# Optimization experiments

Measured on AMD Instinct MI355X. Metric: run time of the kernel, lower is better.

Reference implementation:

```python
import jax, jax.numpy as jnp
import numpy as np

B, L, HID, H, DH = 1, 2048, 1024, 16, 64
KW = 2  # d_conv
EPS = float(np.finfo(np.float32).eps)  # torch RMSNorm eps=None -> dtype eps


def _causal_dw_conv(x, w, b):
    # x: (B, L, D), w: (D, K), b: (D,). Depthwise causal conv, no activation.
    Bs, Ls, D = x.shape
    K = w.shape[1]
    xp = jnp.pad(x, ((0, 0), (K - 1, 0), (0, 0)))
    out = b
    for k in range(K):
        out = out + xp[:, k:k + Ls, :] * w[:, k]
    return out


def setup_inputs() -> dict:
    key = jax.random.key(0)
    ks = jax.random.split(key, 14)
    hidden_states = jax.random.normal(ks[0], (B, L, HID), jnp.float32)
    # masked_fill(attention_mask != 0, -inf): True above diagonal (future masked)
    attention_mask = jnp.triu(jnp.ones((L, L), dtype=bool), 1)[None, None]
    all_dim = 3 * H * DH  # q_size + 2*kv_size with KVH == H
    qkv_w = jax.random.normal(ks[1], (all_dim, HID), jnp.float32) * 0.02
    q_conv_w = jax.random.normal(ks[2], (H * DH, KW), jnp.float32) * 0.5
    q_conv_b = jax.random.normal(ks[3], (H * DH,), jnp.float32) * 0.02
    k_conv_w = jax.random.normal(ks[4], (H * DH, KW), jnp.float32) * 0.5
    k_conv_b = jax.random.normal(ks[5], (H * DH,), jnp.float32) * 0.02
    v_conv_w = jax.random.normal(ks[6], (H * DH, KW), jnp.float32) * 0.5
    v_conv_b = jax.random.normal(ks[7], (H * DH,), jnp.float32) * 0.02
    norm_w = jnp.ones((DH,), jnp.float32)
    A_log = jnp.log(jax.random.uniform(ks[8], (H,), jnp.float32, 1.0, 16.0))
    dt0 = jnp.exp(jax.random.uniform(ks[9], (H,), jnp.float32)
                  * (np.log(0.1) - np.log(0.001)) + np.log(0.001))
    dt0 = jnp.clip(dt0, 1e-4)
    dt_bias = dt0 + jnp.log(-jnp.expm1(-dt0))  # inverse softplus init
    dt_proj_w = jax.random.normal(ks[10], (H, HID), jnp.float32) * 0.02
    dt_proj_b = jnp.zeros((H,), jnp.float32)
    o_w = jax.random.normal(ks[11], (HID, H * DH), jnp.float32) * 0.02
    order_coeff = jnp.ones((1, H, 1, 1), jnp.float32)  # 1/cumprod(arange(1,2))
    return dict(hidden_states=hidden_states, attention_mask=attention_mask,
                qkv_w=qkv_w, q_conv_w=q_conv_w, q_conv_b=q_conv_b,
                k_conv_w=k_conv_w, k_conv_b=k_conv_b, v_conv_w=v_conv_w,
                v_conv_b=v_conv_b, norm_w=norm_w, A_log=A_log, dt_bias=dt_bias,
                dt_proj_w=dt_proj_w, dt_proj_b=dt_proj_b, o_w=o_w,
                order_coeff=order_coeff)


def reference(hidden_states, attention_mask, qkv_w, q_conv_w, q_conv_b,
              k_conv_w, k_conv_b, v_conv_w, v_conv_b, norm_w, A_log, dt_bias,
              dt_proj_w, dt_proj_b, o_w, order_coeff):
    qs = H * DH
    qkv = hidden_states @ qkv_w.T                    # (B, L, 3*H*DH)
    q = _causal_dw_conv(qkv[..., :qs], q_conv_w, q_conv_b)
    k = _causal_dw_conv(qkv[..., qs:2 * qs], k_conv_w, k_conv_b)
    v = _causal_dw_conv(qkv[..., 2 * qs:], v_conv_w, v_conv_b)
    # split heads -> (B, H, L, DH)
    q = q.reshape(B, L, H, DH).transpose(0, 2, 1, 3)
    k = k.reshape(B, L, H, DH).transpose(0, 2, 1, 3)
    v = v.reshape(B, L, H, DH).transpose(0, 2, 1, 3)
    # SSM-style gate: dt (B, L, H)
    dt = jax.nn.softplus(hidden_states @ dt_proj_w.T + dt_proj_b + dt_bias)
    v = v * jnp.swapaxes(dt, 1, 2)[..., None]        # value scaled by dt
    A = -jnp.exp(A_log)[None, None, :] * dt          # (B, L, H)
    A_cumsum = jnp.swapaxes(jnp.cumsum(A, axis=1), 1, 2)  # (B, H, L)
    diff = A_cumsum[:, :, :, None] - A_cumsum[:, :, None, :]  # (B, H, L, L)
    A_mask = jnp.exp(jnp.where(attention_mask, -jnp.inf, diff))
    # order == 1: Taylor series reduces to a single gated linear term
    scores = jnp.einsum('bhld,bhmd->bhlm', q, k) * A_mask * (1.0 / order_coeff)
    out = scores @ v                                  # (B, H, L, DH)
    # RMSNorm over head_dim
    out = out * jax.lax.rsqrt(jnp.mean(out * out, -1, keepdims=True) + EPS) * norm_w
    out = out.transpose(0, 2, 1, 3).reshape(B, L, H * DH)
    return out @ o_w.T
```

## Files before the change

### kernel.cpp

```cpp
#include <hip/hip_runtime.h>
#include <hip/hip_bf16.h>

#define L_SEQ 2048
#define HIDN  1024
#define NH    16
#define DHD   64
#define QKV_N 3072

typedef float f4 __attribute__((ext_vector_type(4)));
typedef __bf16 bf16x8 __attribute__((ext_vector_type(8)));
typedef _Float16 half8 __attribute__((ext_vector_type(8)));
typedef unsigned int u32x2 __attribute__((ext_vector_type(2)));

union H8 {
  half8 h;
  u32x2 u2[2];
  uint4 u4;
};

__device__ __forceinline__ float b2f(unsigned short u) {
  union { unsigned int i; float f; } c; c.i = ((unsigned int)u) << 16; return c.f;
}
__device__ __forceinline__ unsigned short f2b(float f) {
  union { float f; unsigned int i; } c; c.f = f;
  unsigned int r = c.i + 0x7FFFu + ((c.i >> 16) & 1u);
  return (unsigned short)(r >> 16);
}
__device__ __forceinline__ unsigned short f2h(float f) {
  union { _Float16 h; unsigned short u; } c; c.h = (_Float16)f; return c.u;
}
__device__ __forceinline__ void unpack8(uint4 u, float* f) {
  unsigned int w[4] = {u.x, u.y, u.z, u.w};
#pragma unroll
  for (int i = 0; i < 4; ++i) {
    union { unsigned int i_; float f_; } lo, hi;
    lo.i_ = w[i] << 16;
    hi.i_ = w[i] & 0xffff0000u;
    f[2 * i] = lo.f_; f[2 * i + 1] = hi.f_;
  }
}

__global__ void detect_kernel(const unsigned short* __restrict__ hs, int* flag) {
  __shared__ int cnt;
  if (threadIdx.x == 0) cnt = 0;
  __syncthreads();
  int c = 0;
  for (int i = threadIdx.x; i < 8192; i += 256) {
    unsigned int e = (hs[i] >> 7) & 0xFFu;
    if (e >= 140u) c++;
  }
  atomicAdd(&cnt, c);
  __syncthreads();
  if (threadIdx.x == 0) *flag = (cnt >= 32) ? 1 : 0;
}

__global__ __launch_bounds__(256) void convert_big(const void* __restrict__ in,
                                                   unsigned short* __restrict__ out,
                                                   int n, const int* __restrict__ flag) {
  const int i = (blockIdx.x * 256 + threadIdx.x) * 4;
  if (i >= n) return;
  if (*flag) {
    f4 v = *(const f4*)((const float*)in + i);
    ushort4 o;
    o.x = f2b(v[0]); o.y = f2b(v[1]); o.z = f2b(v[2]); o.w = f2b(v[3]);
    *(ushort4*)(out + i) = o;
  } else {
    *(uint2*)(out + i) = *(const uint2*)((const unsigned short*)in + i);
  }
}

__global__ __launch_bounds__(256) void convert_small(
    const void* qw, const void* qb, const void* kw, const void* kb,
    const void* vw, const void* vb, const void* nw, const void* al,
    const void* dtb, const void* dpb, const void* oc,
    float* __restrict__ out, const int* __restrict__ flag) {
  const int f = *flag;
  const void* ptrs[11] = {qw, qb, kw, kb, vw, vb, nw, al, dtb, dpb, oc};
  const int sizes[11] = {2048, 1024, 2048, 1024, 2048, 1024, 64, 16, 16, 16, 16};
  int off = 0;
  for (int a = 0; a < 11; ++a) {
    for (int i = threadIdx.x + blockIdx.x * 256; i < sizes[a]; i += gridDim.x * 256)
      out[off + i] = f ? ((const float*)ptrs[a])[i] : b2f(((const unsigned short*)ptrs[a])[i]);
    off += sizes[a];
  }
}

__global__ __launch_bounds__(256) void gemm128(
    const unsigned short* __restrict__ A, const unsigned short* __restrict__ B,
    float* __restrict__ C, int M, int N, int K)
{
  __shared__ __align__(16) unsigned short As[128 * 40];
  __shared__ __align__(16) unsigned short Bs[128 * 40];
  const int t = threadIdx.x;
  const int w = t >> 6, lane = t & 63;
  const int quad = lane >> 4, l16 = lane & 15;
  const int wr = w >> 1, wc = w & 1;
  const int m0 = blockIdx.y * 128, n0 = blockIdx.x * 128;
  const int srow = t >> 1;
  const int scol = (t & 1) * 16;

  f4 acc[4][4];
#pragma unroll
  for (int i = 0; i < 4; ++i)
#pragma unroll
    for (int j = 0; j < 4; ++j) acc[i][j] = (f4){0.f, 0.f, 0.f, 0.f};

  const unsigned short* apg = A + (size_t)(m0 + srow) * K + scol;
  const unsigned short* bpg = B + (size_t)(n0 + srow) * K + scol;
  uint4 a0 = *(const uint4*)apg,       a1 = *(const uint4*)(apg + 8);
  uint4 b0 = *(const uint4*)bpg,       b1 = *(const uint4*)(bpg + 8);

  for (int k0 = 0; k0 < K; k0 += 32) {
    __syncthreads();
    *(uint4*)&As[srow * 40 + scol]     = a0;
    *(uint4*)&As[srow * 40 + scol + 8] = a1;
    *(uint4*)&Bs[srow * 40 + scol]     = b0;
    *(uint4*)&Bs[srow * 40 + scol + 8] = b1;
    __syncthreads();
    if (k0 + 32 < K) {
      a0 = *(const uint4*)(apg + k0 + 32); a1 = *(const uint4*)(apg + k0 + 40);
      b0 = *(const uint4*)(bpg + k0 + 32); b1 = *(const uint4*)(bpg + k0 + 40);
    }
    bf16x8 aF[4], bF[4];
#pragma unroll
    for (int i = 0; i < 4; ++i)
      aF[i] = *(const bf16x8*)&As[(wr * 64 + i * 16 + l16) * 40 + quad * 8];
#pragma unroll
    for (int j = 0; j < 4; ++j)
      bF[j] = *(const bf16x8*)&Bs[(wc * 64 + j * 16 + l16) * 40 + quad * 8];
#pragma unroll
    for (int i = 0; i < 4; ++i)
#pragma unroll
      for (int j = 0; j < 4; ++j)
        acc[i][j] = __builtin_amdgcn_mfma_f32_16x16x32_bf16(aF[i], bF[j], acc[i][j], 0, 0, 0);
  }

#pragma unroll
  for (int i = 0; i < 4; ++i)
#pragma unroll
    for (int j = 0; j < 4; ++j)
#pragma unroll
      for (int r = 0; r < 4; ++r) {
        int m = m0 + wr * 64 + i * 16 + quad * 4 + r;
        int n = n0 + wc * 64 + j * 16 + l16;
        C[(size_t)m * N + n] = acc[i][j][r];
      }
}

template <int MODE>
__global__ __launch_bounds__(256) void gemm_bt(
    const unsigned short* __restrict__ A, const unsigned short* __restrict__ B,
    void* __restrict__ Cv, int M, int N, int K, const int* __restrict__ flag)
{
  __shared__ __align__(16) short As[64 * 40];
  __shared__ __align__(16) short Bs[64 * 40];
  const int t = threadIdx.x;
  const int wave = t >> 6, lane = t & 63;
  const int quad = lane >> 4, l16 = lane & 15;
  const int m0 = blockIdx.y * 64, n0 = blockIdx.x * 64;
  const int srow = t >> 2, scol = (t & 3) * 8;
  f4 acc[4];
#pragma unroll
  for (int i = 0; i < 4; ++i) acc[i] = (f4){0.f, 0.f, 0.f, 0.f};
  const unsigned short* ap = A + (size_t)(m0 + srow) * K + scol;
  const unsigned short* bp = B + (size_t)(n0 + srow) * K + scol;
  for (int k0 = 0; k0 < K; k0 += 32) {
    uint4 av = *(const uint4*)(ap + k0);
    uint4 bv = *(const uint4*)(bp + k0);
    __syncthreads();
    *(uint4*)&As[srow * 40 + scol] = av;
    *(uint4*)&Bs[srow * 40 + scol] = bv;
    __syncthreads();
    bf16x8 af = *(const bf16x8*)&As[(wave * 16 + l16) * 40 + quad * 8];
#pragma unroll
    for (int nt = 0; nt < 4; ++nt) {
      bf16x8 bf = *(const bf16x8*)&Bs[(nt * 16 + l16) * 40 + quad * 8];
      acc[nt] = __builtin_amdgcn_mfma_f32_16x16x32_bf16(af, bf, acc[nt], 0, 0, 0);
    }
  }
  const int outf32 = (MODE == 0) ? 1 : (*flag ? 1 : 0);
#pragma unroll
  for (int nt = 0; nt < 4; ++nt) {
#pragma unroll
    for (int r = 0; r < 4; ++r) {
      int m = m0 + wave * 16 + quad * 4 + r;
      int n = n0 + nt * 16 + l16;
      if (outf32) ((float*)Cv)[(size_t)m * N + n] = acc[nt][r];
      else        ((unsigned short*)Cv)[(size_t)m * N + n] = f2b(acc[nt][r]);
    }
  }
}

__global__ __launch_bounds__(256) void dt_kernel(
    const unsigned short* __restrict__ hs,
    const unsigned short* __restrict__ dtw,
    const float* __restrict__ smallf,
    float* __restrict__ dt_out, float* __restrict__ A_out)
{
  const int l = blockIdx.x;
  const int t = threadIdx.x, wave = t >> 6, lane = t & 63;
  const unsigned short* hp = hs + (size_t)l * HIDN + lane * 16;
  float hv[16];
  unpack8(*(const uint4*)hp, hv);
  unpack8(*(const uint4*)(hp + 8), hv + 8);
#pragma unroll
  for (int hh = 0; hh < 4; ++hh) {
    const int hd = wave * 4 + hh;
    const unsigned short* wp = dtw + (size_t)hd * HIDN + lane * 16;
    float wv[16];
    unpack8(*(const uint4*)wp, wv);
    unpack8(*(const uint4*)(wp + 8), wv + 8);
    float p = 0.f;
#pragma unroll
    for (int i = 0; i < 16; ++i) p += hv[i] * wv[i];
#pragma unroll
    for (int off = 32; off > 0; off >>= 1) p += __shfl_down(p, off);
    if (lane == 0) {
      float z = p + smallf[9312 + hd] + smallf[9296 + hd];
      float dtv = (z > 20.f) ? z : log1pf(expf(z));
      dt_out[l * NH + hd] = dtv;
      A_out[l * NH + hd] = -expf(smallf[9280 + hd]) * dtv;
    }
  }
}

__global__ __launch_bounds__(64) void cumsum_kernel(const float* __restrict__ A_in,
                                                    float* __restrict__ Ac)
{
  const int h = blockIdx.x;
  const int lane = threadIdx.x;
  const int base = lane * 32;
  float run = 0.f;
  for (int i = 0; i < 32; ++i) run += A_in[(base + i) * NH + h];
  float incl = run;
#pragma unroll
  for (int off = 1; off < 64; off <<= 1) {
    float n = __shfl_up(incl, off);
    if (lane >= off) incl += n;
  }
  float r2 = incl - run;
  for (int i = 0; i < 32; ++i) {
    r2 += A_in[(base + i) * NH + h];
    Ac[h * L_SEQ + base + i] = r2;
  }
}

__global__ __launch_bounds__(256) void conv_kernel(
    const float* __restrict__ qkv, const float* __restrict__ smallf,
    const float* __restrict__ dt, unsigned short* __restrict__ qc)
{
  const int idx = blockIdx.x * 256 + threadIdx.x;
  const int l = idx / (QKV_N / 4);
  const int c = (idx % (QKV_N / 4)) * 4;
  f4 xc = *(const f4*)&qkv[(size_t)l * QKV_N + c];
  f4 xp = (f4){0.f, 0.f, 0.f, 0.f};
  if (l > 0) xp = *(const f4*)&qkv[(size_t)(l - 1) * QKV_N + c];
  const float* w; const float* b; int cb;
  if (c < HIDN)          { w = smallf;        b = smallf + 2048; cb = c; }
  else if (c < 2 * HIDN) { w = smallf + 3072; b = smallf + 5120; cb = c - HIDN; }
  else                   { w = smallf + 6144; b = smallf + 8192; cb = c - 2 * HIDN; }
  f4 o;
#pragma unroll
  for (int j = 0; j < 4; ++j)
    o[j] = b[cb + j] + xp[j] * w[(cb + j) * 2] + xc[j] * w[(cb + j) * 2 + 1];
  if (c >= 2 * HIDN) {
    const int hh = (c - 2 * HIDN) >> 6;
    o *= dt[l * NH + hh];
  }
  ushort4 st;
  st.x = f2h(o[0]); st.y = f2h(o[1]); st.z = f2h(o[2]); st.w = f2h(o[3]);
  *(ushort4*)&qc[(size_t)l * QKV_N + c] = st;
}

__global__ __launch_bounds__(256) void transpose_v(
    const unsigned short* __restrict__ qc, unsigned short* __restrict__ vt)
{
  const int h = blockIdx.y;
  const int l0 = blockIdx.x * 64;
  const int t = threadIdx.x;
  const int srow = t >> 2, cc = t & 3;
  __shared__ __align__(16) unsigned short Ts[64 * 68];
  const unsigned short* gp =
      qc + (size_t)(l0 + srow) * QKV_N + 2 * HIDN + h * DHD + cc * 16;
  uint4 a = *(const uint4*)gp;
  uint4 b = *(const uint4*)(gp + 8);
  *(uint4*)&Ts[srow * 68 + cc * 16] = a;
  *(uint4*)&Ts[srow * 68 + cc * 16 + 8] = b;
  __syncthreads();
  __align__(16) unsigned short o[16];
#pragma unroll
  for (int j = 0; j < 16; ++j) o[j] = Ts[(cc * 16 + j) * 68 + srow];
  unsigned short* op = vt + ((size_t)h * DHD + srow) * L_SEQ + l0 + cc * 16;
  *(uint4*)op = *(const uint4*)&o[0];
  *(uint4*)(op + 8) = *(const uint4*)&o[8];
}

__global__ __launch_bounds__(256) void attn_kernel(
    const unsigned short* __restrict__ qc,
    const unsigned short* __restrict__ vt,
    const float* __restrict__ Ac,
    const float* __restrict__ smallf,
    unsigned short* __restrict__ attn_out)
{
  const int h  = blockIdx.y;
  const int bx = blockIdx.x;
  const int lt = (h < 8) ? (31 - bx) : bx;
  const int t  = threadIdx.x;
  const int w    = t >> 6;
  const int lane = t & 63;
  const int l16  = lane & 15;
  const int quad = lane >> 4;
  const int srow = t >> 2;
  const int cc   = t & 3;

  __shared__ __align__(16) unsigned short K_lds[2][64 * 68];
  __shared__ __align__(16) unsigned short V_lds[2][64 * 68];
  __shared__ __align__(16) unsigned short S_lds[64 * 68];

  const int l0 = lt * 64;
  const float rc = 1.0f / smallf[9328 + h];
  const float* Acp = Ac + h * L_SEQ;

  H8 qf0, qf1;
  {
    const unsigned short* qp =
        qc + (size_t)(l0 + w * 16 + l16) * QKV_N + h * DHD + quad * 8;
    qf0.u4 = *(const uint4*)qp;
    qf1.u4 = *(const uint4*)(qp + 32);
  }
  float alv[4];
#pragma unroll
  for (int r = 0; r < 4; ++r) alv[r] = Acp[l0 + w * 16 + quad * 4 + r];

  f4 acc[4];
#pragma unroll
  for (int i = 0; i < 4; ++i) acc[i] = (f4){0.f, 0.f, 0.f, 0.f};

  const unsigned short* kgp =
      qc + (size_t)srow * QKV_N + HIDN + h * DHD + cc * 16;
  const unsigned short* vgp =
      vt + ((size_t)h * DHD + srow) * L_SEQ + cc * 16;

  const int swo = srow * 68 + cc * 16;

  uint4 k0v = *(const uint4*)kgp,       k1v = *(const uint4*)(kgp + 8);
  uint4 v0v = *(const uint4*)vgp,       v1v = *(const uint4*)(vgp + 8);

  int cur = 0;
  for (int it = 0; it <= lt; ++it) {
    unsigned short* Kl = K_lds[cur];
    unsigned short* Vl = V_lds[cur];
    *(u32x2*)&Kl[swo]      = (u32x2){k0v.x, k0v.y};
    *(u32x2*)&Kl[swo + 4]  = (u32x2){k0v.z, k0v.w};
    *(u32x2*)&Kl[swo + 8]  = (u32x2){k1v.x, k1v.y};
    *(u32x2*)&Kl[swo + 12] = (u32x2){k1v.z, k1v.w};
    *(u32x2*)&Vl[swo]      = (u32x2){v0v.x, v0v.y};
    *(u32x2*)&Vl[swo + 4]  = (u32x2){v0v.z, v0v.w};
    *(u32x2*)&Vl[swo + 8]  = (u32x2){v1v.x, v1v.y};
    *(u32x2*)&Vl[swo + 12] = (u32x2){v1v.z, v1v.w};
    if (it < lt) {
      const unsigned short* kp = kgp + (size_t)(it + 1) * 64 * QKV_N;
      const unsigned short* vp = vgp + (size_t)(it + 1) * 64;
      k0v = *(const uint4*)kp; k1v = *(const uint4*)(kp + 8);
      v0v = *(const uint4*)vp; v1v = *(const uint4*)(vp + 8);
    }
    __syncthreads();

    f4 s[4];
#pragma unroll
    for (int i = 0; i < 4; ++i) s[i] = (f4){0.f, 0.f, 0.f, 0.f};
#pragma unroll
    for (int ks = 0; ks < 2; ++ks) {
      H8 qk = ks ? qf1 : qf0;
#pragma unroll
      for (int nt = 0; nt < 4; ++nt) {
        H8 kf;
        const int ko = (nt * 16 + l16) * 68 + ks * 32 + quad * 8;
        kf.u2[0] = *(const u32x2*)&K_lds[cur][ko];
        kf.u2[1] = *(const u32x2*)&K_lds[cur][ko + 4];
        s[nt] = __builtin_amdgcn_mfma_f32_16x16x32_f16(qk.h, kf.h, s[nt], 0, 0, 0);
      }
    }
    const int m0 = it * 64;
#pragma unroll
    for (int nt = 0; nt < 4; ++nt) {
      const int mg = m0 + nt * 16 + l16;
      const float am = Acp[mg];
#pragma unroll
      for (int r = 0; r < 4; ++r) {
        const int lg = l0 + w * 16 + quad * 4 + r;
        float val = (mg <= lg) ? s[nt][r] * __expf(alv[r] - am) * rc : 0.0f;
        S_lds[(w * 16 + quad * 4 + r) * 68 + nt * 16 + l16] = f2h(val);
      }
    }
#pragma unroll
    for (int ks = 0; ks < 2; ++ks) {
      H8 sa;
      const int so = (w * 16 + l16) * 68 + ks * 32 + quad * 8;
      sa.u2[0] = *(const u32x2*)&S_lds[so];
      sa.u2[1] = *(const u32x2*)&S_lds[so + 4];
#pragma unroll
      for (int db = 0; db < 4; ++db) {
        H8 vb;
        const int vo = (db * 16 + l16) * 68 + ks * 32 + quad * 8;
        vb.u2[0] = *(const u32x2*)&V_lds[cur][vo];
        vb.u2[1] = *(const u32x2*)&V_lds[cur][vo + 4];
        acc[db] = __builtin_amdgcn_mfma_f32_16x16x32_f16(sa.h, vb.h, acc[db], 0, 0, 0);
      }
    }
    cur ^= 1;
  }

#pragma unroll
  for (int r = 0; r < 4; ++r) {
    float p = acc[0][r] * acc[0][r] + acc[1][r] * acc[1][r]
            + acc[2][r] * acc[2][r] + acc[3][r] * acc[3][r];
#pragma unroll
    for (int off = 1; off < 16; off <<= 1) p += __shfl_xor(p, off);
    const float rn = rsqrtf(p * (1.0f / 64.0f) + 1.1920928955078125e-07f);
    unsigned short* op =
        attn_out + (size_t)(l0 + w * 16 + quad * 4 + r) * HIDN + h * DHD + l16;
#pragma unroll
    for (int ds = 0; ds < 4; ++ds)
      op[ds * 16] = f2b(acc[ds][r] * rn * smallf[9216 + ds * 16 + l16]);
  }
}

extern "C" void kernel_launch(void* const* d_in, const int* in_sizes, int n_in,
                              void* d_out, int out_size, void* d_ws, size_t ws_size,
                              hipStream_t stream)
{
  (void)in_sizes; (void)n_in; (void)out_size; (void)ws_size;
  const void* hs        = d_in[0];
  const void* qkv_w     = d_in[2];
  const void* q_conv_w  = d_in[3];
  const void* q_conv_b  = d_in[4];
  const void* k_conv_w  = d_in[5];
  const void* k_conv_b  = d_in[6];
  const void* v_conv_w  = d_in[7];
  const void* v_conv_b  = d_in[8];
  const void* norm_w    = d_in[9];
  const void* A_log     = d_in[10];
  const void* dt_bias   = d_in[11];
  const void* dt_proj_w = d_in[12];
  const void* dt_proj_b = d_in[13];
  const void* o_w       = d_in[14];
  const void* ordc      = d_in[15];

  char* ws = (char*)d_ws;
  int* flag             = (int*)ws;
  unsigned short* hs_b  = (unsigned short*)(ws + 256);
  unsigned short* qkvw_b= (unsigned short*)(ws + 4194560);
  unsigned short* ow_b  = (unsigned short*)(ws + 10486016);
  unsigned short* dtw_b = (unsigned short*)(ws + 12583168);
  float* smallf         = (float*)(ws + 12615936);
  float* qkv            = (float*)(ws + 12653568);
  unsigned short* qc_h  = (unsigned short*)(ws + 37819392);
  float* dtbuf          = (float*)(ws + 62985216);
  float* Abuf           = (float*)(ws + 63116288);
  float* Acum           = (float*)(ws + 63247360);
  unsigned short* attnb = (unsigned short*)(ws + 63378432);
  unsigned short* vt_h  = (unsigned short*)(ws + 67572736);

  detect_kernel<<<1, 256, 0, stream>>>((const unsigned short*)hs, flag);
  convert_big<<<(2097152 / 4 + 255) / 256, 256, 0, stream>>>(hs, hs_b, 2097152, flag);
  convert_big<<<(3145728 / 4 + 255) / 256, 256, 0, stream>>>(qkv_w, qkvw_b, 3145728, flag);
  convert_big<<<(1048576 / 4 + 255) / 256, 256, 0, stream>>>(o_w, ow_b, 1048576, flag);
  convert_big<<<(16384 / 4 + 255) / 256, 256, 0, stream>>>(dt_proj_w, dtw_b, 16384, flag);
  convert_small<<<4, 256, 0, stream>>>(q_conv_w, q_conv_b, k_conv_w, k_conv_b,
                                       v_conv_w, v_conv_b, norm_w, A_log,
                                       dt_bias, dt_proj_b, ordc, smallf, flag);

  gemm128<<<dim3(QKV_N / 128, L_SEQ / 128), 256, 0, stream>>>(
      hs_b, qkvw_b, qkv, L_SEQ, QKV_N, HIDN);
  dt_kernel<<<L_SEQ, 256, 0, stream>>>(hs_b, dtw_b, smallf, dtbuf, Abuf);
  cumsum_kernel<<<NH, 64, 0, stream>>>(Abuf, Acum);
  conv_kernel<<<(L_SEQ * QKV_N / 4) / 256, 256, 0, stream>>>(qkv, smallf, dtbuf, qc_h);
  transpose_v<<<dim3(L_SEQ / 64, NH), 256, 0, stream>>>(qc_h, vt_h);
  attn_kernel<<<dim3(32, NH), 256, 0, stream>>>(qc_h, vt_h, Acum, smallf, attnb);
  gemm_bt<1><<<dim3(HIDN / 64, L_SEQ / 64), 256, 0, stream>>>(
      attnb, ow_b, d_out, L_SEQ, HIDN, HIDN, flag);
}
```

Baseline: 257.1 us.

## Fuse prep kernels into one launch and restructure attention double-buffering

Merges the dtype-detect kernel, four bulk conversion launches and the small-parameter conversion into one grid-stride prep kernel. Each block redoes the dtype detection itself, which removes five launches and the serialization between them at the cost of repeated reads. In the attention kernel, the next K/V tile's LDS stores now happen after the compute, with one barrier per iteration, and the A_cumsum values are prefetched in registers. Tile order alternates between long and short causal rows to balance block load.

New measurement: 244.0 us. -5.1%, faster.

```diff
diff --git a/kernel.cpp b/kernel.cpp
--- a/kernel.cpp
+++ b/kernel.cpp
@@ -40,47 +40,54 @@
   }
 }
 
-__global__ void detect_kernel(const unsigned short* __restrict__ hs, int* flag) {
+__global__ __launch_bounds__(256) void prep_kernel(
+    const void* hs, const void* qkvw, const void* ow, const void* dtw,
+    const void* qw, const void* qb, const void* kw, const void* kb,
+    const void* vw, const void* vb, const void* nw, const void* al,
+    const void* dtb, const void* dpb, const void* oc,
+    unsigned short* __restrict__ hs_b, unsigned short* __restrict__ qkvw_b,
+    unsigned short* __restrict__ ow_b, unsigned short* __restrict__ dtw_b,
+    float* __restrict__ smallf, int* __restrict__ flag)
+{
   __shared__ int cnt;
   if (threadIdx.x == 0) cnt = 0;
   __syncthreads();
-  int c = 0;
-  for (int i = threadIdx.x; i < 8192; i += 256) {
-    unsigned int e = (hs[i] >> 7) & 0xFFu;
-    if (e >= 140u) c++;
-  }
-  atomicAdd(&cnt, c);
+  {
+    const unsigned short* p = (const unsigned short*)hs;
+    int c = 0;
+    for (int i = threadIdx.x; i < 8192; i += 256)
+      if (((p[i] >> 7) & 0xFFu) >= 140u) c++;
+    atomicAdd(&cnt, c);
+  }
   __syncthreads();
-  if (threadIdx.x == 0) *flag = (cnt >= 32) ? 1 : 0;
-}
-
-__global__ __launch_bounds__(256) void convert_big(const void* __restrict__ in,
-                                                   unsigned short* __restrict__ out,
-                                                   int n, const int* __restrict__ flag) {
-  const int i = (blockIdx.x * 256 + threadIdx.x) * 4;
-  if (i >= n) return;
-  if (*flag) {
-    f4 v = *(const f4*)((const float*)in + i);
-    ushort4 o;
-    o.x = f2b(v[0]); o.y = f2b(v[1]); o.z = f2b(v[2]); o.w = f2b(v[3]);
-    *(ushort4*)(out + i) = o;
-  } else {
-    *(uint2*)(out + i) = *(const uint2*)((const unsigned short*)in + i);
-  }
-}
-
-__global__ __launch_bounds__(256) void convert_small(
-    const void* qw, const void* qb, const void* kw, const void* kb,
-    const void* vw, const void* vb, const void* nw, const void* al,
-    const void* dtb, const void* dpb, const void* oc,
-    float* __restrict__ out, const int* __restrict__ flag) {
-  const int f = *flag;
+  const int f = (cnt >= 32) ? 1 : 0;
+  if (blockIdx.x == 0 && threadIdx.x == 0) *flag = f;
+
+  const int tid = blockIdx.x * 256 + threadIdx.x;
+  const int nth = gridDim.x * 256;
+  for (int i = tid; i < 1576960; i += nth) {
+    const void* src; unsigned short* dst; int off;
+    if (i < 524288)       { src = hs;   dst = hs_b;   off = i; }
+    else if (i < 1310720) { src = qkvw; dst = qkvw_b; off = i - 524288; }
+    else if (i < 1572864) { src = ow;   dst = ow_b;   off = i - 1310720; }
+    else                  { src = dtw;  dst = dtw_b;  off = i - 1572864; }
+    const int e = off * 4;
+    if (f) {
+      f4 v = *(const f4*)((const float*)src + e);
+      ushort4 o;
+      o.x = f2b(v[0]); o.y = f2b(v[1]); o.z = f2b(v[2]); o.w = f2b(v[3]);
+      *(ushort4*)(dst + e) = o;
+    } else {
+      *(uint2*)(dst + e) = *(const uint2*)((const unsigned short*)src + e);
+    }
+  }
   const void* ptrs[11] = {qw, qb, kw, kb, vw, vb, nw, al, dtb, dpb, oc};
   const int sizes[11] = {2048, 1024, 2048, 1024, 2048, 1024, 64, 16, 16, 16, 16};
   int off = 0;
   for (int a = 0; a < 11; ++a) {
-    for (int i = threadIdx.x + blockIdx.x * 256; i < sizes[a]; i += gridDim.x * 256)
-      out[off + i] = f ? ((const float*)ptrs[a])[i] : b2f(((const unsigned short*)ptrs[a])[i]);
+    for (int i = tid; i < sizes[a]; i += nth)
+      smallf[off + i] = f ? ((const float*)ptrs[a])[i]
+                          : b2f(((const unsigned short*)ptrs[a])[i]);
     off += sizes[a];
   }
 }
@@ -304,7 +311,9 @@
 {
   const int h  = blockIdx.y;
   const int bx = blockIdx.x;
-  const int lt = (h < 8) ? (31 - bx) : bx;
+  const int jj = bx >> 1;
+  const int base = (bx & 1) ? jj : (31 - jj);
+  const int lt = (h < 8) ? base : (31 - base);
   const int t  = threadIdx.x;
   const int w    = t >> 6;
   const int lane = t & 63;
@@ -345,26 +354,34 @@
 
   uint4 k0v = *(const uint4*)kgp,       k1v = *(const uint4*)(kgp + 8);
   uint4 v0v = *(const uint4*)vgp,       v1v = *(const uint4*)(vgp + 8);
+  float amv[4];
+#pragma unroll
+  for (int nt = 0; nt < 4; ++nt) amv[nt] = Acp[nt * 16 + l16];
+
+  *(u32x2*)&K_lds[0][swo]      = (u32x2){k0v.x, k0v.y};
+  *(u32x2*)&K_lds[0][swo + 4]  = (u32x2){k0v.z, k0v.w};
+  *(u32x2*)&K_lds[0][swo + 8]  = (u32x2){k1v.x, k1v.y};
+  *(u32x2*)&K_lds[0][swo + 12] = (u32x2){k1v.z, k1v.w};
+  *(u32x2*)&V_lds[0][swo]      = (u32x2){v0v.x, v0v.y};
+  *(u32x2*)&V_lds[0][swo + 4]  = (u32x2){v0v.z, v0v.w};
+  *(u32x2*)&V_lds[0][swo + 8]  = (u32x2){v1v.x, v1v.y};
+  *(u32x2*)&V_lds[0][swo + 12] = (u32x2){v1v.z, v1v.w};
+  __syncthreads();
 
   int cur = 0;
   for (int it = 0; it <= lt; ++it) {
-    unsigned short* Kl = K_lds[cur];
-    unsigned short* Vl = V_lds[cur];
-    *(u32x2*)&Kl[swo]      = (u32x2){k0v.x, k0v.y};
-    *(u32x2*)&Kl[swo + 4]  = (u32x2){k0v.z, k0v.w};
-    *(u32x2*)&Kl[swo + 8]  = (u32x2){k1v.x, k1v.y};
-    *(u32x2*)&Kl[swo + 12] = (u32x2){k1v.z, k1v.w};
-    *(u32x2*)&Vl[swo]      = (u32x2){v0v.x, v0v.y};
-    *(u32x2*)&Vl[swo + 4]  = (u32x2){v0v.z, v0v.w};
-    *(u32x2*)&Vl[swo + 8]  = (u32x2){v1v.x, v1v.y};
-    *(u32x2*)&Vl[swo + 12] = (u32x2){v1v.z, v1v.w};
-    if (it < lt) {
+    uint4 nk0 = k0v, nk1 = k1v, nv0 = v0v, nv1 = v1v;
+    float namv[4];
+    const bool more = (it < lt);
+    if (more) {
       const unsigned short* kp = kgp + (size_t)(it + 1) * 64 * QKV_N;
       const unsigned short* vp = vgp + (size_t)(it + 1) * 64;
-      k0v = *(const uint4*)kp; k1v = *(const uint4*)(kp + 8);
-      v0v = *(const uint4*)vp; v1v = *(const uint4*)(vp + 8);
-    }
-    __syncthreads();
+      nk0 = *(const uint4*)kp; nk1 = *(const uint4*)(kp + 8);
+      nv0 = *(const uint4*)vp; nv1 = *(const uint4*)(vp + 8);
+#pragma unroll
+      for (int nt = 0; nt < 4; ++nt)
+        namv[nt] = Acp[(it + 1) * 64 + nt * 16 + l16];
+    }
 
     f4 s[4];
 #pragma unroll
@@ -385,7 +402,7 @@
 #pragma unroll
     for (int nt = 0; nt < 4; ++nt) {
       const int mg = m0 + nt * 16 + l16;
-      const float am = Acp[mg];
+      const float am = amv[nt];
 #pragma unroll
       for (int r = 0; r < 4; ++r) {
         const int lg = l0 + w * 16 + quad * 4 + r;
@@ -408,7 +425,22 @@
         acc[db] = __builtin_amdgcn_mfma_f32_16x16x32_f16(sa.h, vb.h, acc[db], 0, 0, 0);
       }
     }
-    cur ^= 1;
+    if (more) {
+      unsigned short* Kl = K_lds[cur ^ 1];
+      unsigned short* Vl = V_lds[cur ^ 1];
+      *(u32x2*)&Kl[swo]      = (u32x2){nk0.x, nk0.y};
+      *(u32x2*)&Kl[swo + 4]  = (u32x2){nk0.z, nk0.w};
+      *(u32x2*)&Kl[swo + 8]  = (u32x2){nk1.x, nk1.y};
+      *(u32x2*)&Kl[swo + 12] = (u32x2){nk1.z, nk1.w};
+      *(u32x2*)&Vl[swo]      = (u32x2){nv0.x, nv0.y};
+      *(u32x2*)&Vl[swo + 4]  = (u32x2){nv0.z, nv0.w};
+      *(u32x2*)&Vl[swo + 8]  = (u32x2){nv1.x, nv1.y};
+      *(u32x2*)&Vl[swo + 12] = (u32x2){nv1.z, nv1.w};
+#pragma unroll
+      for (int nt = 0; nt < 4; ++nt) amv[nt] = namv[nt];
+      __syncthreads();
+      cur ^= 1;
+    }
   }
 
 #pragma unroll
@@ -462,14 +494,11 @@
   unsigned short* attnb = (unsigned short*)(ws + 63378432);
   unsigned short* vt_h  = (unsigned short*)(ws + 67572736);
 
-  detect_kernel<<<1, 256, 0, stream>>>((const unsigned short*)hs, flag);
-  convert_big<<<(2097152 / 4 + 255) / 256, 256, 0, stream>>>(hs, hs_b, 2097152, flag);
-  convert_big<<<(3145728 / 4 + 255) / 256, 256, 0, stream>>>(qkv_w, qkvw_b, 3145728, flag);
-  convert_big<<<(1048576 / 4 + 255) / 256, 256, 0, stream>>>(o_w, ow_b, 1048576, flag);
-  convert_big<<<(16384 / 4 + 255) / 256, 256, 0, stream>>>(dt_proj_w, dtw_b, 16384, flag);
-  convert_small<<<4, 256, 0, stream>>>(q_conv_w, q_conv_b, k_conv_w, k_conv_b,
-                                       v_conv_w, v_conv_b, norm_w, A_log,
-                                       dt_bias, dt_proj_b, ordc, smallf, flag);
+  prep_kernel<<<1024, 256, 0, stream>>>(
+      hs, qkv_w, o_w, dt_proj_w,
+      q_conv_w, q_conv_b, k_conv_w, k_conv_b, v_conv_w, v_conv_b,
+      norm_w, A_log, dt_bias, dt_proj_b, ordc,
+      hs_b, qkvw_b, ow_b, dtw_b, smallf, flag);
 
   gemm128<<<dim3(QKV_N / 128, L_SEQ / 128), 256, 0, stream>>>(
       hs_b, qkvw_b, qkv, L_SEQ, QKV_N, HIDN);
```
